# Kernel tuning notes

Hardware: AMD Instinct MI355X
Metric: run time of the kernel (lower is better)

## Reference

```python
import jax, jax.numpy as jnp
import numpy as np

DIM = 1536
NHEADS = 12
HDIM = DIM // NHEADS  # 128
EPS = 1e-6
LOCAL_ATTN_SIZE = 3
SINK_SIZE = 1
MAX_ATTN = 32760 if LOCAL_ATTN_SIZE == -1 else LOCAL_ATTN_SIZE * 1560  # 4680


def _rms(x, g):
    # WanRMSNorm over last dim
    return x * jax.lax.rsqrt(jnp.mean(x * x, axis=-1, keepdims=True) + EPS) * g


def _rope(x, f, h, w, fr, fi, start_frame):
    # x: [b, s, n, d] with s == f*h*w; fr/fi: [1024, d//2] real/imag of complex rotations
    b, s, n, d = x.shape
    c = d // 2
    c0 = c - 2 * (c // 3)
    c1 = c // 3
    fc = jax.lax.complex(fr, fi)  # [1024, c]
    xr = x.reshape(b, s, n, c, 2)
    xc = jax.lax.complex(xr[..., 0], xr[..., 1])  # [b, s, n, c]
    ff = fc[start_frame:start_frame + f, :c0]      # [f, c0]
    fh = fc[:h, c0:c0 + c1]                        # [h, c1]
    fw = fc[:w, c0 + c1:c0 + 2 * c1]               # [w, c1]
    freqs_i = jnp.concatenate([
        jnp.broadcast_to(ff[:, None, None, :], (f, h, w, c0)),
        jnp.broadcast_to(fh[None, :, None, :], (f, h, w, c1)),
        jnp.broadcast_to(fw[None, None, :, :], (f, h, w, c1)),
    ], axis=-1).reshape(1, s, 1, c)
    y = xc * freqs_i
    return jnp.stack([y.real, y.imag], axis=-1).reshape(b, s, n, d)


def _attn(q, k, v):
    # plain SDPA (decode path of the module uses no mask on the gathered window)
    scale = 1.0 / np.sqrt(q.shape[-1]).astype(np.float32)
    logits = jnp.einsum('bqnd,bknd->bnqk', q, k) * scale
    p = jax.nn.softmax(logits, axis=-1)
    return jnp.einsum('bnqk,bknd->bqnd', p, v)


def _forward(x, cache_k, cache_v, freqs_real, freqs_imag,
             wq, bq, wk, bk, wv, bv, wo, bo, gq, gk,
             f_frames, height, width, current_start, global_end_index, local_end_index):
    b, s, _ = x.shape
    n, d = NHEADS, HDIM
    frame_seqlen = height * width
    start_frame = current_start // frame_seqlen

    q = _rms(x @ wq + bq, gq).reshape(b, s, n, d)
    k = _rms(x @ wk + bk, gk).reshape(b, s, n, d)
    v = (x @ wv + bv).reshape(b, s, n, d)

    rq = _rope(q, f_frames, height, width, freqs_real, freqs_imag, start_frame)
    rk = _rope(k, f_frames, height, width, freqs_real, freqs_imag, start_frame)

    current_end = current_start + s
    sink_tokens = SINK_SIZE * frame_seqlen
    kv_size = cache_k.shape[1]
    is_recompute = (current_end <= global_end_index) and (current_start > 0)

    kc, vc = cache_k, cache_v
    if LOCAL_ATTN_SIZE != -1 and current_end > global_end_index and s + local_end_index > kv_size:
        # evict oldest non-sink tokens, roll the rest toward the sink region
        num_evicted = s + local_end_index - kv_size
        num_rolled = local_end_index - num_evicted - sink_tokens
        src = slice(sink_tokens + num_evicted, sink_tokens + num_evicted + num_rolled)
        kc = kc.at[:, sink_tokens:sink_tokens + num_rolled].set(jax.lax.stop_gradient(cache_k[:, src]))
        vc = vc.at[:, sink_tokens:sink_tokens + num_rolled].set(jax.lax.stop_gradient(cache_v[:, src]))
        new_local_end = local_end_index + current_end - global_end_index - num_evicted
    else:
        new_local_end = local_end_index + current_end - global_end_index
    local_start = new_local_end - s
    write_start = max(local_start, sink_tokens) if is_recompute else local_start
    off = max(0, write_start - local_start)
    wl = max(0, new_local_end - write_start)
    if wl > 0:
        kc = kc.at[:, write_start:new_local_end].set(rk[:, off:off + wl])
        vc = vc.at[:, write_start:new_local_end].set(v[:, off:off + wl])

    if sink_tokens > 0:
        budget = MAX_ATTN - sink_tokens
        if budget > 0:
            lo = max(sink_tokens, new_local_end - budget)
            kcat = jnp.concatenate([kc[:, :sink_tokens], kc[:, lo:new_local_end]], axis=1)
            vcat = jnp.concatenate([vc[:, :sink_tokens], vc[:, lo:new_local_end]], axis=1)
        else:
            kcat, vcat = kc[:, :sink_tokens], vc[:, :sink_tokens]
        o = _attn(rq, kcat, vcat)
    else:
        ws = max(0, new_local_end - MAX_ATTN)
        o = _attn(rq, kc[:, ws:new_local_end], vc[:, ws:new_local_end])

    return o.reshape(b, s, DIM) @ wo + bo


def setup_inputs() -> dict:
    key = jax.random.key(0)
    ks = jax.random.split(key, 12)
    B, S, CACHE = 1, 1560, 4680
    sc = 0.02
    # RoPE tables as unit-magnitude complex rotations
    ang = jax.random.uniform(ks[0], (1024, HDIM // 2), jnp.float32, 0.0, 2.0 * np.pi)
    return {
        'x': jax.random.normal(ks[1], (B, S, DIM), jnp.float32),
        'cache_k': jax.random.normal(ks[2], (B, CACHE, NHEADS, HDIM), jnp.float32),
        'cache_v': jax.random.normal(ks[3], (B, CACHE, NHEADS, HDIM), jnp.float32),
        'freqs_real': jnp.cos(ang),
        'freqs_imag': jnp.sin(ang),
        'wq': jax.random.normal(ks[4], (DIM, DIM), jnp.float32) * sc,
        'bq': jnp.zeros((DIM,), jnp.float32),
        'wk': jax.random.normal(ks[5], (DIM, DIM), jnp.float32) * sc,
        'bk': jnp.zeros((DIM,), jnp.float32),
        'wv': jax.random.normal(ks[6], (DIM, DIM), jnp.float32) * sc,
        'bv': jnp.zeros((DIM,), jnp.float32),
        'wo': jax.random.normal(ks[7], (DIM, DIM), jnp.float32) * sc,
        'bo': jnp.zeros((DIM,), jnp.float32),
        'gq': jnp.ones((DIM,), jnp.float32),
        'gk': jnp.ones((DIM,), jnp.float32),
        'f_frames': 1,
        'height': 30,
        'width': 52,
        'current_start': 4680,
        'global_end_index': 4680,
        'local_end_index': 4680,
    }


def reference(x, cache_k, cache_v, freqs_real, freqs_imag,
              wq, bq, wk, bk, wv, bv, wo, bo, gq, gk,
              f_frames, height, width, current_start, global_end_index, local_end_index):
    return _forward(x, cache_k, cache_v, freqs_real, freqs_imag,
                    wq, bq, wk, bk, wv, bv, wo, bo, gq, gk,
                    f_frames, height, width, current_start, global_end_index, local_end_index)
```

## Files before the change

kernel.cpp:

```cpp
#include <hip/hip_runtime.h>
#include <cstdint>
#include <cstddef>

typedef unsigned int  u32;
typedef unsigned short u16;
typedef short s16x8 __attribute__((ext_vector_type(8)));
typedef float f32x4 __attribute__((ext_vector_type(4)));

#define DIM     1536
#define NH      12
#define HD      128
#define SEQ     1560
#define MPAD    1664
#define NKV     4680
#define NKPAD   4736
#define ROLL0   3120
#define NQK     4608
#define START_FRAME 3
#define NEGINF  -3.0e4f
#define NSPLIT  4
#define SPLITKC 1216

__device__ __forceinline__ u16 f2bf(float f){
  u32 u = __builtin_bit_cast(u32, f);
  u32 r = (u + 0x7fffu + ((u >> 16) & 1u)) >> 16;
  return (u16)r;
}

__global__ void k_pre(const float* __restrict__ x, u16* __restrict__ xp,
                      u16* __restrict__ Kc, u16* __restrict__ VT,
                      u16* __restrict__ Qr, u16* __restrict__ Opad,
                      float* __restrict__ sumsq){
  int b = blockIdx.x;
  if (b < 244){
    int i = b * 256 + threadIdx.x;
    uint4 z = make_uint4(0u, 0u, 0u, 0u);
    if (i < 10752){
      int h = i / 896, r = i % 896;
      ((uint4*)(Kc + ((size_t)h * NKPAD + NKV) * 128))[r] = z;
    } else if (i < 21504){
      int j = i - 10752; int row = j / 7, c = j % 7;
      ((uint4*)(VT + (size_t)row * NKPAD + NKV))[c] = z;
    } else if (i < 41472){
      int j = i - 21504; int h = j / 1664, r = j % 1664;
      ((uint4*)(Qr + ((size_t)h * MPAD + SEQ) * 128))[r] = z;
    } else if (i < 61440){
      int r = i - 41472;
      ((uint4*)(Opad + (size_t)SEQ * DIM))[r] = z;
    } else if (i < 62272){
      ((uint4*)sumsq)[i - 61440] = z;
    }
  } else {
    int i = (b - 244) * 256 + threadIdx.x;
    const int n_src = SEQ * DIM / 8;
    u16 o[8] = {0,0,0,0,0,0,0,0};
    if (i < n_src){
      float4 a = ((const float4*)x)[2*i];
      float4 c = ((const float4*)x)[2*i + 1];
      o[0]=f2bf(a.x); o[1]=f2bf(a.y); o[2]=f2bf(a.z); o[3]=f2bf(a.w);
      o[4]=f2bf(c.x); o[5]=f2bf(c.y); o[6]=f2bf(c.z); o[7]=f2bf(c.w);
    }
    uint4 v = make_uint4((u32)o[0]|((u32)o[1]<<16), (u32)o[2]|((u32)o[3]<<16),
                         (u32)o[4]|((u32)o[5]<<16), (u32)o[6]|((u32)o[7]<<16));
    ((uint4*)xp)[i] = v;
  }
}

__global__ void k_transpose_w(const float* __restrict__ wq, const float* __restrict__ wk,
                              const float* __restrict__ wv, const float* __restrict__ wo,
                              u16* __restrict__ WTqkv, u16* __restrict__ WTo){
  __shared__ u32 tile[64][65];
  int z = blockIdx.z;
  const float* w = (z==0)?wq:(z==1)?wk:(z==2)?wv:wo;
  u16* dst = (z < 3) ? (WTqkv + (size_t)z * DIM * DIM) : WTo;
  int r0 = blockIdx.x * 64, c0 = blockIdx.y * 64;
  int t = threadIdx.x;
  int rr = t >> 4, cg = t & 15;
#pragma unroll
  for (int i = 0; i < 4; i++){
    int r = rr + i * 16;
    float4 v = *(const float4*)(w + (size_t)(r0 + r) * DIM + c0 + cg * 4);
    tile[r][cg*4+0] = f2bf(v.x); tile[r][cg*4+1] = f2bf(v.y);
    tile[r][cg*4+2] = f2bf(v.z); tile[r][cg*4+3] = f2bf(v.w);
  }
  __syncthreads();
  int c = t >> 2, rg = t & 3;
  u32 wds[8];
#pragma unroll
  for (int j = 0; j < 8; j++)
    wds[j] = (tile[rg*16 + 2*j][c] & 0xffffu) | (tile[rg*16 + 2*j + 1][c] << 16);
  u16* q = dst + (size_t)(c0 + c) * DIM + r0 + rg * 16;
  *(uint4*)q       = make_uint4(wds[0], wds[1], wds[2], wds[3]);
  *(uint4*)(q + 8) = make_uint4(wds[4], wds[5], wds[6], wds[7]);
}

#define LDK 40
__global__ __launch_bounds__(256) void k_gemm_qkv(
    const u16* __restrict__ A, const u16* __restrict__ B,
    const float* __restrict__ biasq, const float* __restrict__ biask, const float* __restrict__ biasv,
    float* __restrict__ Y, float* __restrict__ sumsq){
  __shared__ u16 As[128*LDK];
  __shared__ u16 Bs[128*LDK];
  int m0 = blockIdx.y * 128, n0 = blockIdx.x * 128;
  int t = threadIdx.x, w = t >> 6, lane = t & 63, quad = lane >> 4, lc = lane & 15;
  int wm = w & 1, wn = w >> 1;
  int sr = t >> 1, sh = (t & 1) * 16;
  f32x4 acc[4][4] = {};
  for (int kt = 0; kt < DIM/32; kt++){
    int k0 = kt * 32;
    __syncthreads();
    {
      const uint4* ga = (const uint4*)(A + (size_t)(m0 + sr) * DIM + k0 + sh);
      uint4 a0 = ga[0], a1 = ga[1];
      const uint4* gb = (const uint4*)(B + (size_t)(n0 + sr) * DIM + k0 + sh);
      uint4 b0 = gb[0], b1 = gb[1];
      *(uint4*)(As + sr * LDK + sh)     = a0;
      *(uint4*)(As + sr * LDK + sh + 8) = a1;
      *(uint4*)(Bs + sr * LDK + sh)     = b0;
      *(uint4*)(Bs + sr * LDK + sh + 8) = b1;
    }
    __syncthreads();
    s16x8 af[4], bf[4];
#pragma unroll
    for (int mt = 0; mt < 4; mt++) af[mt] = *(const s16x8*)(As + (wm*64 + mt*16 + lc) * LDK + quad * 8);
#pragma unroll
    for (int nt = 0; nt < 4; nt++) bf[nt] = *(const s16x8*)(Bs + (wn*64 + nt*16 + lc) * LDK + quad * 8);
#pragma unroll
    for (int mt = 0; mt < 4; mt++)
#pragma unroll
      for (int nt = 0; nt < 4; nt++)
        acc[mt][nt] = __builtin_amdgcn_mfma_f32_16x16x32_bf16(af[mt], bf[nt], acc[mt][nt], 0, 0, 0);
  }
  const float* bias; int cbase; int which;
  if (n0 < DIM)        { bias = biasq; cbase = 0;     which = 0; }
  else if (n0 < 2*DIM) { bias = biask; cbase = DIM;   which = 1; }
  else                 { bias = biasv; cbase = 2*DIM; which = 2; }
  float bvals[4];
#pragma unroll
  for (int nt = 0; nt < 4; nt++) bvals[nt] = bias[n0 - cbase + wn*64 + nt*16 + lc];
#pragma unroll
  for (int mt = 0; mt < 4; mt++){
    int row0 = m0 + wm*64 + mt*16 + quad*4;
    float ss[4] = {0.f, 0.f, 0.f, 0.f};
#pragma unroll
    for (int nt = 0; nt < 4; nt++){
      int col = n0 + wn*64 + nt*16 + lc;
#pragma unroll
      for (int r = 0; r < 4; r++){
        float y = acc[mt][nt][r] + bvals[nt];
        Y[(size_t)(row0 + r) * NQK + col] = y;
        ss[r] += y * y;
      }
    }
    if (which < 2){
      float* dst = sumsq + (which ? MPAD : 0);
#pragma unroll
      for (int r = 0; r < 4; r++){
        float v = ss[r];
        v += __shfl_xor(v, 1); v += __shfl_xor(v, 2); v += __shfl_xor(v, 4); v += __shfl_xor(v, 8);
        if (lc == 0) atomicAdd(&dst[row0 + r], v);
      }
    }
  }
}

__global__ void k_rope_qk(const float* __restrict__ Y, const float* __restrict__ sumsq,
                          const float* __restrict__ gq, const float* __restrict__ gk,
                          const float* __restrict__ fre, const float* __restrict__ fim,
                          u16* __restrict__ Qr, u16* __restrict__ Kc){
  int pos = blockIdx.x;
  int t = threadIdx.x;
  float scq = rsqrtf(sumsq[pos]        * (1.0f/1536.0f) + 1e-6f);
  float sck = rsqrtf(sumsq[MPAD + pos] * (1.0f/1536.0f) + 1e-6f);
  int hrow = pos / 52, wrow = pos % 52;
#pragma unroll
  for (int i = 0; i < 3; i++){
    int p = t + i * 256;
    int head = p >> 6, j = p & 63;
    int frow = (j < 22) ? START_FRAME : ((j < 43) ? hrow : wrow);
    float cr = fre[frow * 64 + j], ci = fim[frow * 64 + j];
    int d0 = head * 128 + 2 * j;
    float2 yq = *(const float2*)(Y + (size_t)pos * NQK + d0);
    float qa = yq.x * scq * gq[d0];
    float qb = yq.y * scq * gq[d0 + 1];
    u32 oq = (u32)f2bf(qa * cr - qb * ci) | ((u32)f2bf(qa * ci + qb * cr) << 16);
    *(u32*)(Qr + (size_t)(head * MPAD + pos) * 128 + 2 * j) = oq;
    float2 yk = *(const float2*)(Y + (size_t)pos * NQK + DIM + d0);
    float ka = yk.x * sck * gk[d0];
    float kb = yk.y * sck * gk[d0 + 1];
    u32 ok = (u32)f2bf(ka * cr - kb * ci) | ((u32)f2bf(ka * ci + kb * cr) << 16);
    *(u32*)(Kc + (size_t)(head * NKPAD + ROLL0 + pos) * 128 + 2 * j) = ok;
  }
}

__global__ void k_copy_cache_k(const float* __restrict__ ck, u16* __restrict__ Kc){
  int p = blockIdx.x;
  int src = (p < SEQ) ? p : p + SEQ;
  int t = threadIdx.x;
  int h = t >> 4, d = (t & 15) * 8;
  const float* s = ck + (size_t)src * DIM + t * 8;
  float4 a = ((const float4*)s)[0], b = ((const float4*)s)[1];
  uint4 v = make_uint4((u32)f2bf(a.x)|((u32)f2bf(a.y)<<16), (u32)f2bf(a.z)|((u32)f2bf(a.w)<<16),
                       (u32)f2bf(b.x)|((u32)f2bf(b.y)<<16), (u32)f2bf(b.z)|((u32)f2bf(b.w)<<16));
  *(uint4*)(Kc + (size_t)(h * NKPAD + p) * 128 + d) = v;
}

__global__ void k_tv_cache(const float* __restrict__ cv, u16* __restrict__ VT){
  __shared__ u32 tile[64][65];
  int p0 = blockIdx.x * 64, hd0 = blockIdx.y * 64;
  int t = threadIdx.x;
  int pr = t >> 4, cg = t & 15;
#pragma unroll
  for (int i = 0; i < 4; i++){
    int p = p0 + pr + i * 16;
    if (p < ROLL0){
      int src = (p < SEQ) ? p : p + SEQ;
      float4 v = *(const float4*)(cv + (size_t)src * DIM + hd0 + cg * 4);
      tile[pr + i*16][cg*4+0] = f2bf(v.x); tile[pr + i*16][cg*4+1] = f2bf(v.y);
      tile[pr + i*16][cg*4+2] = f2bf(v.z); tile[pr + i*16][cg*4+3] = f2bf(v.w);
    }
  }
  __syncthreads();
  int hd = t >> 2, pg = t & 3;
  int pbase = p0 + pg * 16;
  if (pbase < ROLL0){
    u32 wds[8];
#pragma unroll
    for (int j = 0; j < 8; j++)
      wds[j] = (tile[pg*16 + 2*j][hd] & 0xffffu) | (tile[pg*16 + 2*j + 1][hd] << 16);
    u16* q = VT + (size_t)(hd0 + hd) * NKPAD + pbase;
    *(uint4*)q       = make_uint4(wds[0], wds[1], wds[2], wds[3]);
    *(uint4*)(q + 8) = make_uint4(wds[4], wds[5], wds[6], wds[7]);
  }
}

__global__ void k_tv_new(const float* __restrict__ Y, u16* __restrict__ VT){
  __shared__ u32 tile[64][65];
  int p0 = blockIdx.x * 64, hd0 = blockIdx.y * 64;
  int t = threadIdx.x;
  int pr = t >> 4, cg = t & 15;
#pragma unroll
  for (int i = 0; i < 4; i++){
    int p = p0 + pr + i * 16;
    if (p < SEQ){
      float4 v = *(const float4*)(Y + (size_t)p * NQK + 2*DIM + hd0 + cg * 4);
      tile[pr + i*16][cg*4+0] = f2bf(v.x); tile[pr + i*16][cg*4+1] = f2bf(v.y);
      tile[pr + i*16][cg*4+2] = f2bf(v.z); tile[pr + i*16][cg*4+3] = f2bf(v.w);
    }
  }
  __syncthreads();
  int hd = t >> 2, pg = t & 3;
  int pbase = p0 + pg * 16;
  u32 wds[8];
#pragma unroll
  for (int j = 0; j < 8; j++)
    wds[j] = (tile[pg*16 + 2*j][hd] & 0xffffu) | (tile[pg*16 + 2*j + 1][hd] << 16);
  u16* q = VT + (size_t)(hd0 + hd) * NKPAD + ROLL0 + pbase;
  if (pbase + 8  <= SEQ) *(uint4*)q       = make_uint4(wds[0], wds[1], wds[2], wds[3]);
  if (pbase + 16 <= SEQ) *(uint4*)(q + 8) = make_uint4(wds[4], wds[5], wds[6], wds[7]);
}

#define DEFER_THR 8.0f
__global__ __launch_bounds__(512, 4) void k_attn(const u16* __restrict__ Qr, const u16* __restrict__ Kc,
                                                 const u16* __restrict__ VT,
                                                 float* __restrict__ Opart, float* __restrict__ ml){
  __shared__ u16 Ks[64 * 128];
  __shared__ u16 Vs[128 * 64];
  int h = blockIdx.y, qb = blockIdx.x, sp = blockIdx.z;
  int t = threadIdx.x, w = t >> 6, lane = t & 63, quad = lane >> 4, lc = lane & 15;
  int qbase = qb * 128 + w * 16;
  const u16* Qbase = Qr + (size_t)(h * MPAD + qbase + lc) * 128;
  s16x8 qf[4];
#pragma unroll
  for (int kk = 0; kk < 4; kk++) qf[kk] = *(const s16x8*)(Qbase + kk * 32 + quad * 8);
  f32x4 oacc[8] = {};
  float m_ = NEGINF;
  float l_ = 0.f;
  const float scale = 0.08838834764831845f;
  const u16* Kh = Kc + (size_t)h * NKPAD * 128;
  const u16* Vh = VT + (size_t)h * 128 * NKPAD;
  int kr0 = t >> 4,          kg0 = (t & 15) * 8;
  int kr1 = (t + 512) >> 4,  kg1 = ((t + 512) & 15) * 8;
  int vd0 = t >> 3,          vp0 = (t & 7) * 8;
  int vd1 = (t + 512) >> 3,  vp1 = ((t + 512) & 7) * 8;
  int ksw0 = kr0 * 128 + (kg0 ^ ((kr0 & 7) << 3));
  int ksw1 = kr1 * 128 + (kg1 ^ ((kr1 & 7) << 3));
  int vsw0 = vd0 * 64  + (vp0 ^ ((vd0 & 7) << 3));
  int vsw1 = vd1 * 64  + (vp1 ^ ((vd1 & 7) << 3));
  int xork = (lc & 7) << 3;
  int aa = (lc + ((quad & 1) << 5)) << 2;
  int ab = aa + 64;
  int hi = quad >> 1;

  int kc0 = sp * SPLITKC;
  int kc1 = (sp == NSPLIT-1) ? NKPAD : kc0 + SPLITKC;
  uint4 kp0, kp1, vq0, vq1;
  {
    int kc = kc0;
    kp0 = *(const uint4*)(Kh + (size_t)(kc + kr0) * 128 + kg0);
    kp1 = *(const uint4*)(Kh + (size_t)(kc + kr1) * 128 + kg1);
    vq0 = *(const uint4*)(Vh + (size_t)vd0 * NKPAD + kc + vp0);
    vq1 = *(const uint4*)(Vh + (size_t)vd1 * NKPAD + kc + vp1);
  }
  for (int kc = kc0; kc < kc1; kc += 64){
    __syncthreads();
    *(uint4*)(Ks + ksw0) = kp0;
    *(uint4*)(Ks + ksw1) = kp1;
    *(uint4*)(Vs + vsw0) = vq0;
    *(uint4*)(Vs + vsw1) = vq1;
    __syncthreads();
    if (kc + 64 < kc1){
      int kn = kc + 64;
      kp0 = *(const uint4*)(Kh + (size_t)(kn + kr0) * 128 + kg0);
      kp1 = *(const uint4*)(Kh + (size_t)(kn + kr1) * 128 + kg1);
      vq0 = *(const uint4*)(Vh + (size_t)vd0 * NKPAD + kn + vp0);
      vq1 = *(const uint4*)(Vh + (size_t)vd1 * NKPAD + kn + vp1);
    }
    float s[4][4];
    __builtin_amdgcn_s_setprio(1);
#pragma unroll
    for (int nt = 0; nt < 4; nt++){
      f32x4 acc = {};
      int p = nt * 16 + lc;
#pragma unroll
      for (int kk = 0; kk < 4; kk++){
        s16x8 kf = *(const s16x8*)(Ks + p * 128 + (((kk * 4 + quad) * 8) ^ xork));
        acc = __builtin_amdgcn_mfma_f32_16x16x32_bf16(kf, qf[kk], acc, 0, 0, 0);
      }
#pragma unroll
      for (int r = 0; r < 4; r++) s[nt][r] = acc[r] * scale;
    }
    __builtin_amdgcn_s_setprio(0);
    if (kc + 64 > NKV){
#pragma unroll
      for (int nt = 0; nt < 4; nt++){
        int keyb = kc + nt * 16 + quad * 4;
#pragma unroll
        for (int r = 0; r < 4; r++) if (keyb + r >= NKV) s[nt][r] = NEGINF;
      }
    }
    float mx = fmaxf(fmaxf(s[0][0], s[0][1]), fmaxf(s[0][2], s[0][3]));
#pragma unroll
    for (int nt = 1; nt < 4; nt++)
      mx = fmaxf(mx, fmaxf(fmaxf(s[nt][0], s[nt][1]), fmaxf(s[nt][2], s[nt][3])));
    mx = fmaxf(mx, __shfl_xor(mx, 16));
    mx = fmaxf(mx, __shfl_xor(mx, 32));
    if (__any(mx > m_ + DEFER_THR)){
      float mnew = fmaxf(m_, mx);
      float alpha = __expf(m_ - mnew);
      m_ = mnew; l_ *= alpha;
      float alr[4];
#pragma unroll
      for (int r = 0; r < 4; r++) alr[r] = __shfl(alpha, quad * 4 + r);
#pragma unroll
      for (int dt = 0; dt < 8; dt++){
        f32x4 oo = oacc[dt];
#pragma unroll
        for (int r = 0; r < 4; r++) oo[r] *= alr[r];
        oacc[dt] = oo;
      }
    }
#pragma unroll
    for (int nt = 0; nt < 4; nt++)
#pragma unroll
      for (int r = 0; r < 4; r++) s[nt][r] = __expf(s[nt][r] - m_);
    float sum = (s[0][0] + s[0][1]) + (s[0][2] + s[0][3]);
#pragma unroll
    for (int nt = 1; nt < 4; nt++)
      sum += (s[nt][0] + s[nt][1]) + (s[nt][2] + s[nt][3]);
    sum += __shfl_xor(sum, 16);
    sum += __shfl_xor(sum, 32);
    l_ += sum;
    u32 w01[4], w23[4];
#pragma unroll
    for (int nt = 0; nt < 4; nt++){
      w01[nt] = (u32)f2bf(s[nt][0]) | ((u32)f2bf(s[nt][1]) << 16);
      w23[nt] = (u32)f2bf(s[nt][2]) | ((u32)f2bf(s[nt][3]) << 16);
    }
    u32 x0, x1;
    uint4 A0, A1;
    x0 = (u32)__builtin_amdgcn_ds_bpermute(aa, (int)w01[0]);
    x1 = (u32)__builtin_amdgcn_ds_bpermute(aa, (int)w01[1]);
    A0.x = hi ? x1 : x0;
    x0 = (u32)__builtin_amdgcn_ds_bpermute(aa, (int)w23[0]);
    x1 = (u32)__builtin_amdgcn_ds_bpermute(aa, (int)w23[1]);
    A0.y = hi ? x1 : x0;
    x0 = (u32)__builtin_amdgcn_ds_bpermute(ab, (int)w01[0]);
    x1 = (u32)__builtin_amdgcn_ds_bpermute(ab, (int)w01[1]);
    A0.z = hi ? x1 : x0;
    x0 = (u32)__builtin_amdgcn_ds_bpermute(ab, (int)w23[0]);
    x1 = (u32)__builtin_amdgcn_ds_bpermute(ab, (int)w23[1]);
    A0.w = hi ? x1 : x0;
    x0 = (u32)__builtin_amdgcn_ds_bpermute(aa, (int)w01[2]);
    x1 = (u32)__builtin_amdgcn_ds_bpermute(aa, (int)w01[3]);
    A1.x = hi ? x1 : x0;
    x0 = (u32)__builtin_amdgcn_ds_bpermute(aa, (int)w23[2]);
    x1 = (u32)__builtin_amdgcn_ds_bpermute(aa, (int)w23[3]);
    A1.y = hi ? x1 : x0;
    x0 = (u32)__builtin_amdgcn_ds_bpermute(ab, (int)w01[2]);
    x1 = (u32)__builtin_amdgcn_ds_bpermute(ab, (int)w01[3]);
    A1.z = hi ? x1 : x0;
    x0 = (u32)__builtin_amdgcn_ds_bpermute(ab, (int)w23[2]);
    x1 = (u32)__builtin_amdgcn_ds_bpermute(ab, (int)w23[3]);
    A1.w = hi ? x1 : x0;
    s16x8 a0 = __builtin_bit_cast(s16x8, A0);
    s16x8 a1 = __builtin_bit_cast(s16x8, A1);
    __builtin_amdgcn_s_setprio(1);
#pragma unroll
    for (int dt = 0; dt < 8; dt++){
      int d = dt * 16 + lc;
      s16x8 v0 = *(const s16x8*)(Vs + d * 64 + ((quad * 8) ^ xork));
      s16x8 v1 = *(const s16x8*)(Vs + d * 64 + ((32 + quad * 8) ^ xork));
      oacc[dt] = __builtin_amdgcn_mfma_f32_16x16x32_bf16(a0, v0, oacc[dt], 0, 0, 0);
      oacc[dt] = __builtin_amdgcn_mfma_f32_16x16x32_bf16(a1, v1, oacc[dt], 0, 0, 0);
    }
    __builtin_amdgcn_s_setprio(0);
  }
  float mr[4], lr[4];
#pragma unroll
  for (int r = 0; r < 4; r++){
    mr[r] = __shfl(m_, quad * 4 + r);
    lr[r] = __shfl(l_, quad * 4 + r);
  }
  float* Ob = Opart + ((size_t)(sp * NH + h) * SEQ) * 128;
  float* mlb = ml + ((size_t)(sp * NH + h) * SEQ) * 2;
#pragma unroll
  for (int dt = 0; dt < 8; dt++)
#pragma unroll
    for (int r = 0; r < 4; r++){
      int row = qbase + quad * 4 + r;
      if (row < SEQ) Ob[(size_t)row * 128 + dt * 16 + lc] = oacc[dt][r];
    }
  if (lc == 0){
#pragma unroll
    for (int r = 0; r < 4; r++){
      int row = qbase + quad * 4 + r;
      if (row < SEQ){
        mlb[row * 2 + 0] = mr[r];
        mlb[row * 2 + 1] = lr[r];
      }
    }
  }
}

__global__ void k_attn_cmb(const float* __restrict__ Opart, const float* __restrict__ ml,
                           u16* __restrict__ Og){
  int row = blockIdx.x, h = blockIdx.y, d = threadIdx.x;
  float m[NSPLIT], l[NSPLIT];
  float M = NEGINF;
#pragma unroll
  for (int s = 0; s < NSPLIT; s++){
    m[s] = ml[((size_t)(s * NH + h) * SEQ + row) * 2 + 0];
    l[s] = ml[((size_t)(s * NH + h) * SEQ + row) * 2 + 1];
    M = fmaxf(M, m[s]);
  }
  float L = 0.f, o = 0.f;
#pragma unroll
  for (int s = 0; s < NSPLIT; s++){
    float wgt = __expf(m[s] - M);
    L += wgt * l[s];
    o += wgt * Opart[((size_t)(s * NH + h) * SEQ + row) * 128 + d];
  }
  Og[(size_t)row * DIM + h * 128 + d] = f2bf(o / L);
}

__global__ __launch_bounds__(256) void k_gemm_out(const u16* __restrict__ A, const u16* __restrict__ B,
                                                  const float* __restrict__ bo, float* __restrict__ out){
  __shared__ u16 As[128*LDK];
  __shared__ u16 Bs[128*LDK];
  int m0 = blockIdx.y * 128, n0 = blockIdx.x * 128;
  int t = threadIdx.x, w = t >> 6, lane = t & 63, quad = lane >> 4, lc = lane & 15;
  int wm = w & 1, wn = w >> 1;
  int sr = t >> 1, sh = (t & 1) * 16;
  f32x4 acc[4][4] = {};
  for (int kt = 0; kt < DIM/32; kt++){
    int k0 = kt * 32;
    __syncthreads();
    {
      const uint4* ga = (const uint4*)(A + (size_t)(m0 + sr) * DIM + k0 + sh);
      uint4 a0 = ga[0], a1 = ga[1];
      const uint4* gb = (const uint4*)(B + (size_t)(n0 + sr) * DIM + k0 + sh);
      uint4 b0 = gb[0], b1 = gb[1];
      *(uint4*)(As + sr * LDK + sh)     = a0;
      *(uint4*)(As + sr * LDK + sh + 8) = a1;
      *(uint4*)(Bs + sr * LDK + sh)     = b0;
      *(uint4*)(Bs + sr * LDK + sh + 8) = b1;
    }
    __syncthreads();
    s16x8 af[4], bf[4];
#pragma unroll
    for (int mt = 0; mt < 4; mt++) af[mt] = *(const s16x8*)(As + (wm*64 + mt*16 + lc) * LDK + quad * 8);
#pragma unroll
    for (int nt = 0; nt < 4; nt++) bf[nt] = *(const s16x8*)(Bs + (wn*64 + nt*16 + lc) * LDK + quad * 8);
#pragma unroll
    for (int mt = 0; mt < 4; mt++)
#pragma unroll
      for (int nt = 0; nt < 4; nt++)
        acc[mt][nt] = __builtin_amdgcn_mfma_f32_16x16x32_bf16(af[mt], bf[nt], acc[mt][nt], 0, 0, 0);
  }
  float bvals[4];
#pragma unroll
  for (int nt = 0; nt < 4; nt++) bvals[nt] = bo[n0 + wn*64 + nt*16 + lc];
#pragma unroll
  for (int mt = 0; mt < 4; mt++){
    int row0 = m0 + wm*64 + mt*16 + quad*4;
#pragma unroll
    for (int nt = 0; nt < 4; nt++){
      int col = n0 + wn*64 + nt*16 + lc;
#pragma unroll
      for (int r = 0; r < 4; r++){
        int row = row0 + r;
        if (row < SEQ) out[(size_t)row * DIM + col] = acc[mt][nt][r] + bvals[nt];
      }
    }
  }
}

extern "C" void kernel_launch(void* const* d_in, const int* in_sizes, int n_in,
                              void* d_out, int out_size, void* d_ws, size_t ws_size,
                              hipStream_t stream){
  const float* x   = (const float*)d_in[0];
  const float* ck  = (const float*)d_in[1];
  const float* cv  = (const float*)d_in[2];
  const float* fre = (const float*)d_in[3];
  const float* fim = (const float*)d_in[4];
  const float* wq  = (const float*)d_in[5];
  const float* bq  = (const float*)d_in[6];
  const float* wk  = (const float*)d_in[7];
  const float* bk  = (const float*)d_in[8];
  const float* wv  = (const float*)d_in[9];
  const float* bv  = (const float*)d_in[10];
  const float* wo  = (const float*)d_in[11];
  const float* bo  = (const float*)d_in[12];
  const float* gq  = (const float*)d_in[13];
  const float* gk  = (const float*)d_in[14];

  char* ws = (char*)d_ws;
  size_t off = 0;
  u16*   xpad  = (u16*)(ws + off);  off += (size_t)MPAD * DIM * 2;
  u16*   WTqkv = (u16*)(ws + off);  off += (size_t)3 * DIM * DIM * 2;
  float* Y     = (float*)(ws + off); off += (size_t)MPAD * NQK * 4;
  u16*   WTo   = (u16*)(ws + off);  off += (size_t)DIM * DIM * 2;
  float* sumsq = (float*)(ws + off); off += (size_t)2 * MPAD * 4;
  u16*   Qr    = (u16*)(ws + off);  off += (size_t)NH * MPAD * 128 * 2;
  u16*   Kc    = (u16*)(ws + off);  off += (size_t)NH * NKPAD * 128 * 2;
  u16*   VT    = (u16*)(ws + off);  off += (size_t)NH * 128 * NKPAD * 2;
  u16*   Opad  = (u16*)(ws + off);  off += (size_t)MPAD * DIM * 2;
  if (off > ws_size) return;
  float* Opart = (float*)ws;
  float* ml    = (float*)(ws + (size_t)NSPLIT * NH * SEQ * 128 * 4);

  k_pre         <<<dim3(1492), 256, 0, stream>>>(x, xpad, Kc, VT, Qr, Opad, sumsq);
  k_transpose_w <<<dim3(24, 24, 4), 256, 0, stream>>>(wq, wk, wv, wo, WTqkv, WTo);
  k_gemm_qkv    <<<dim3(NQK/128, MPAD/128), 256, 0, stream>>>(xpad, WTqkv, bq, bk, bv, Y, sumsq);
  k_rope_qk     <<<dim3(SEQ), 256, 0, stream>>>(Y, sumsq, gq, gk, fre, fim, Qr, Kc);
  k_copy_cache_k<<<dim3(ROLL0), 192, 0, stream>>>(ck, Kc);
  k_tv_cache    <<<dim3(49, 24), 256, 0, stream>>>(cv, VT);
  k_tv_new      <<<dim3(25, 24), 256, 0, stream>>>(Y, VT);
  k_attn        <<<dim3(MPAD/128, NH, NSPLIT), 512, 0, stream>>>(Qr, Kc, VT, Opart, ml);
  k_attn_cmb    <<<dim3(SEQ, NH), 128, 0, stream>>>(Opart, ml, Opad);
  k_gemm_out    <<<dim3(DIM/128, MPAD/128), 256, 0, stream>>>(Opad, WTo, bo, (float*)d_out);
}
```

Measured before the change: 377.3 us.

## Process two query sub-tiles per wave in attention to reuse K/V fragments

The attention kernel now runs 256 threads per block, and each wave handles 32 query rows as two 16-row sub-tiles (A and B) instead of one. Each K fragment and V fragment read from LDS feeds two MFMAs, which halves LDS reads per MFMA and gives each wave more independent MFMA work. In exchange, accumulator and softmax register state doubles, launch bounds drop to (256,2), and each block stages its K/V tile with half as many threads. Occupancy falls and register spills become a risk.

After: 519.7 us. 37.8% more time.

```diff
diff --git a/kernel.cpp b/kernel.cpp
--- a/kernel.cpp
+++ b/kernel.cpp
@@ -261,32 +261,38 @@
 }
 
 #define DEFER_THR 8.0f
-__global__ __launch_bounds__(512, 4) void k_attn(const u16* __restrict__ Qr, const u16* __restrict__ Kc,
+__global__ __launch_bounds__(256, 2) void k_attn(const u16* __restrict__ Qr, const u16* __restrict__ Kc,
                                                  const u16* __restrict__ VT,
                                                  float* __restrict__ Opart, float* __restrict__ ml){
   __shared__ u16 Ks[64 * 128];
   __shared__ u16 Vs[128 * 64];
   int h = blockIdx.y, qb = blockIdx.x, sp = blockIdx.z;
   int t = threadIdx.x, w = t >> 6, lane = t & 63, quad = lane >> 4, lc = lane & 15;
-  int qbase = qb * 128 + w * 16;
-  const u16* Qbase = Qr + (size_t)(h * MPAD + qbase + lc) * 128;
-  s16x8 qf[4];
-#pragma unroll
-  for (int kk = 0; kk < 4; kk++) qf[kk] = *(const s16x8*)(Qbase + kk * 32 + quad * 8);
-  f32x4 oacc[8] = {};
-  float m_ = NEGINF;
-  float l_ = 0.f;
+  int qbaseA = qb * 128 + w * 32;
+  int qbaseB = qbaseA + 16;
+  const u16* QbA = Qr + (size_t)(h * MPAD + qbaseA + lc) * 128;
+  const u16* QbB = Qr + (size_t)(h * MPAD + qbaseB + lc) * 128;
+  s16x8 qfA[4], qfB[4];
+#pragma unroll
+  for (int kk = 0; kk < 4; kk++){
+    qfA[kk] = *(const s16x8*)(QbA + kk * 32 + quad * 8);
+    qfB[kk] = *(const s16x8*)(QbB + kk * 32 + quad * 8);
+  }
+  f32x4 oaccA[8] = {}, oaccB[8] = {};
+  float mA = NEGINF, lA = 0.f;
+  float mB = NEGINF, lB = 0.f;
   const float scale = 0.08838834764831845f;
   const u16* Kh = Kc + (size_t)h * NKPAD * 128;
   const u16* Vh = VT + (size_t)h * 128 * NKPAD;
-  int kr0 = t >> 4,          kg0 = (t & 15) * 8;
-  int kr1 = (t + 512) >> 4,  kg1 = ((t + 512) & 15) * 8;
-  int vd0 = t >> 3,          vp0 = (t & 7) * 8;
-  int vd1 = (t + 512) >> 3,  vp1 = ((t + 512) & 7) * 8;
-  int ksw0 = kr0 * 128 + (kg0 ^ ((kr0 & 7) << 3));
-  int ksw1 = kr1 * 128 + (kg1 ^ ((kr1 & 7) << 3));
-  int vsw0 = vd0 * 64  + (vp0 ^ ((vd0 & 7) << 3));
-  int vsw1 = vd1 * 64  + (vp1 ^ ((vd1 & 7) << 3));
+  int kr[4], kg[4], ksw[4], vd[4], vp[4], vsw[4];
+#pragma unroll
+  for (int i = 0; i < 4; i++){
+    int n = t + i * 256;
+    kr[i] = n >> 4;  kg[i] = (n & 15) * 8;
+    ksw[i] = kr[i] * 128 + (kg[i] ^ ((kr[i] & 7) << 3));
+    vd[i] = n >> 3;  vp[i] = (n & 7) * 8;
+    vsw[i] = vd[i] * 64 + (vp[i] ^ ((vd[i] & 7) << 3));
+  }
   int xork = (lc & 7) << 3;
   int aa = (lc + ((quad & 1) << 5)) << 2;
   int ab = aa + 64;
@@ -294,41 +300,45 @@
 
   int kc0 = sp * SPLITKC;
   int kc1 = (sp == NSPLIT-1) ? NKPAD : kc0 + SPLITKC;
-  uint4 kp0, kp1, vq0, vq1;
-  {
-    int kc = kc0;
-    kp0 = *(const uint4*)(Kh + (size_t)(kc + kr0) * 128 + kg0);
-    kp1 = *(const uint4*)(Kh + (size_t)(kc + kr1) * 128 + kg1);
-    vq0 = *(const uint4*)(Vh + (size_t)vd0 * NKPAD + kc + vp0);
-    vq1 = *(const uint4*)(Vh + (size_t)vd1 * NKPAD + kc + vp1);
+  uint4 kp[4], vq[4];
+#pragma unroll
+  for (int i = 0; i < 4; i++){
+    kp[i] = *(const uint4*)(Kh + (size_t)(kc0 + kr[i]) * 128 + kg[i]);
+    vq[i] = *(const uint4*)(Vh + (size_t)vd[i] * NKPAD + kc0 + vp[i]);
   }
   for (int kc = kc0; kc < kc1; kc += 64){
     __syncthreads();
-    *(uint4*)(Ks + ksw0) = kp0;
-    *(uint4*)(Ks + ksw1) = kp1;
-    *(uint4*)(Vs + vsw0) = vq0;
-    *(uint4*)(Vs + vsw1) = vq1;
+#pragma unroll
+    for (int i = 0; i < 4; i++){
+      *(uint4*)(Ks + ksw[i]) = kp[i];
+      *(uint4*)(Vs + vsw[i]) = vq[i];
+    }
     __syncthreads();
     if (kc + 64 < kc1){
       int kn = kc + 64;
-      kp0 = *(const uint4*)(Kh + (size_t)(kn + kr0) * 128 + kg0);
-      kp1 = *(const uint4*)(Kh + (size_t)(kn + kr1) * 128 + kg1);
-      vq0 = *(const uint4*)(Vh + (size_t)vd0 * NKPAD + kn + vp0);
-      vq1 = *(const uint4*)(Vh + (size_t)vd1 * NKPAD + kn + vp1);
-    }
-    float s[4][4];
+#pragma unroll
+      for (int i = 0; i < 4; i++){
+        kp[i] = *(const uint4*)(Kh + (size_t)(kn + kr[i]) * 128 + kg[i]);
+        vq[i] = *(const uint4*)(Vh + (size_t)vd[i] * NKPAD + kn + vp[i]);
+      }
+    }
+    float sA[4][4], sB[4][4];
     __builtin_amdgcn_s_setprio(1);
 #pragma unroll
     for (int nt = 0; nt < 4; nt++){
-      f32x4 acc = {};
+      f32x4 accA = {}, accB = {};
       int p = nt * 16 + lc;
 #pragma unroll
       for (int kk = 0; kk < 4; kk++){
         s16x8 kf = *(const s16x8*)(Ks + p * 128 + (((kk * 4 + quad) * 8) ^ xork));
-        acc = __builtin_amdgcn_mfma_f32_16x16x32_bf16(kf, qf[kk], acc, 0, 0, 0);
-      }
-#pragma unroll
-      for (int r = 0; r < 4; r++) s[nt][r] = acc[r] * scale;
+        accA = __builtin_amdgcn_mfma_f32_16x16x32_bf16(kf, qfA[kk], accA, 0, 0, 0);
+        accB = __builtin_amdgcn_mfma_f32_16x16x32_bf16(kf, qfB[kk], accB, 0, 0, 0);
+      }
+#pragma unroll
+      for (int r = 0; r < 4; r++){
+        sA[nt][r] = accA[r] * scale;
+        sB[nt][r] = accB[r] * scale;
+      }
     }
     __builtin_amdgcn_s_setprio(0);
     if (kc + 64 > NKV){
@@ -336,91 +346,136 @@
       for (int nt = 0; nt < 4; nt++){
         int keyb = kc + nt * 16 + quad * 4;
 #pragma unroll
-        for (int r = 0; r < 4; r++) if (keyb + r >= NKV) s[nt][r] = NEGINF;
-      }
-    }
-    float mx = fmaxf(fmaxf(s[0][0], s[0][1]), fmaxf(s[0][2], s[0][3]));
-#pragma unroll
-    for (int nt = 1; nt < 4; nt++)
-      mx = fmaxf(mx, fmaxf(fmaxf(s[nt][0], s[nt][1]), fmaxf(s[nt][2], s[nt][3])));
-    mx = fmaxf(mx, __shfl_xor(mx, 16));
-    mx = fmaxf(mx, __shfl_xor(mx, 32));
-    if (__any(mx > m_ + DEFER_THR)){
-      float mnew = fmaxf(m_, mx);
-      float alpha = __expf(m_ - mnew);
-      m_ = mnew; l_ *= alpha;
-      float alr[4];
-#pragma unroll
-      for (int r = 0; r < 4; r++) alr[r] = __shfl(alpha, quad * 4 + r);
+        for (int r = 0; r < 4; r++)
+          if (keyb + r >= NKV){ sA[nt][r] = NEGINF; sB[nt][r] = NEGINF; }
+      }
+    }
+    float mxA = fmaxf(fmaxf(sA[0][0], sA[0][1]), fmaxf(sA[0][2], sA[0][3]));
+    float mxB = fmaxf(fmaxf(sB[0][0], sB[0][1]), fmaxf(sB[0][2], sB[0][3]));
+#pragma unroll
+    for (int nt = 1; nt < 4; nt++){
+      mxA = fmaxf(mxA, fmaxf(fmaxf(sA[nt][0], sA[nt][1]), fmaxf(sA[nt][2], sA[nt][3])));
+      mxB = fmaxf(mxB, fmaxf(fmaxf(sB[nt][0], sB[nt][1]), fmaxf(sB[nt][2], sB[nt][3])));
+    }
+    mxA = fmaxf(mxA, __shfl_xor(mxA, 16));  mxB = fmaxf(mxB, __shfl_xor(mxB, 16));
+    mxA = fmaxf(mxA, __shfl_xor(mxA, 32));  mxB = fmaxf(mxB, __shfl_xor(mxB, 32));
+    if (__any((mxA > mA + DEFER_THR) || (mxB > mB + DEFER_THR))){
+      float mnA = fmaxf(mA, mxA), mnB = fmaxf(mB, mxB);
+      float alA = __expf(mA - mnA), alB = __expf(mB - mnB);
+      mA = mnA; lA *= alA;  mB = mnB; lB *= alB;
+      float arA[4], arB[4];
+#pragma unroll
+      for (int r = 0; r < 4; r++){
+        arA[r] = __shfl(alA, quad * 4 + r);
+        arB[r] = __shfl(alB, quad * 4 + r);
+      }
 #pragma unroll
       for (int dt = 0; dt < 8; dt++){
-        f32x4 oo = oacc[dt];
-#pragma unroll
-        for (int r = 0; r < 4; r++) oo[r] *= alr[r];
-        oacc[dt] = oo;
+        f32x4 oA = oaccA[dt], oB = oaccB[dt];
+#pragma unroll
+        for (int r = 0; r < 4; r++){ oA[r] *= arA[r]; oB[r] *= arB[r]; }
+        oaccA[dt] = oA; oaccB[dt] = oB;
       }
     }
 #pragma unroll
     for (int nt = 0; nt < 4; nt++)
 #pragma unroll
-      for (int r = 0; r < 4; r++) s[nt][r] = __expf(s[nt][r] - m_);
-    float sum = (s[0][0] + s[0][1]) + (s[0][2] + s[0][3]);
-#pragma unroll
-    for (int nt = 1; nt < 4; nt++)
-      sum += (s[nt][0] + s[nt][1]) + (s[nt][2] + s[nt][3]);
-    sum += __shfl_xor(sum, 16);
-    sum += __shfl_xor(sum, 32);
-    l_ += sum;
-    u32 w01[4], w23[4];
+      for (int r = 0; r < 4; r++){
+        sA[nt][r] = __expf(sA[nt][r] - mA);
+        sB[nt][r] = __expf(sB[nt][r] - mB);
+      }
+    float smA = (sA[0][0] + sA[0][1]) + (sA[0][2] + sA[0][3]);
+    float smB = (sB[0][0] + sB[0][1]) + (sB[0][2] + sB[0][3]);
+#pragma unroll
+    for (int nt = 1; nt < 4; nt++){
+      smA += (sA[nt][0] + sA[nt][1]) + (sA[nt][2] + sA[nt][3]);
+      smB += (sB[nt][0] + sB[nt][1]) + (sB[nt][2] + sB[nt][3]);
+    }
+    smA += __shfl_xor(smA, 16);  smB += __shfl_xor(smB, 16);
+    smA += __shfl_xor(smA, 32);  smB += __shfl_xor(smB, 32);
+    lA += smA;  lB += smB;
+    u32 a01[4], a23[4], b01[4], b23[4];
 #pragma unroll
     for (int nt = 0; nt < 4; nt++){
-      w01[nt] = (u32)f2bf(s[nt][0]) | ((u32)f2bf(s[nt][1]) << 16);
-      w23[nt] = (u32)f2bf(s[nt][2]) | ((u32)f2bf(s[nt][3]) << 16);
+      a01[nt] = (u32)f2bf(sA[nt][0]) | ((u32)f2bf(sA[nt][1]) << 16);
+      a23[nt] = (u32)f2bf(sA[nt][2]) | ((u32)f2bf(sA[nt][3]) << 16);
+      b01[nt] = (u32)f2bf(sB[nt][0]) | ((u32)f2bf(sB[nt][1]) << 16);
+      b23[nt] = (u32)f2bf(sB[nt][2]) | ((u32)f2bf(sB[nt][3]) << 16);
     }
     u32 x0, x1;
-    uint4 A0, A1;
-    x0 = (u32)__builtin_amdgcn_ds_bpermute(aa, (int)w01[0]);
-    x1 = (u32)__builtin_amdgcn_ds_bpermute(aa, (int)w01[1]);
+    uint4 A0, A1, B0, B1;
+    x0 = (u32)__builtin_amdgcn_ds_bpermute(aa, (int)a01[0]);
+    x1 = (u32)__builtin_amdgcn_ds_bpermute(aa, (int)a01[1]);
     A0.x = hi ? x1 : x0;
-    x0 = (u32)__builtin_amdgcn_ds_bpermute(aa, (int)w23[0]);
-    x1 = (u32)__builtin_amdgcn_ds_bpermute(aa, (int)w23[1]);
+    x0 = (u32)__builtin_amdgcn_ds_bpermute(aa, (int)a23[0]);
+    x1 = (u32)__builtin_amdgcn_ds_bpermute(aa, (int)a23[1]);
     A0.y = hi ? x1 : x0;
-    x0 = (u32)__builtin_amdgcn_ds_bpermute(ab, (int)w01[0]);
-    x1 = (u32)__builtin_amdgcn_ds_bpermute(ab, (int)w01[1]);
+    x0 = (u32)__builtin_amdgcn_ds_bpermute(ab, (int)a01[0]);
+    x1 = (u32)__builtin_amdgcn_ds_bpermute(ab, (int)a01[1]);
     A0.z = hi ? x1 : x0;
-    x0 = (u32)__builtin_amdgcn_ds_bpermute(ab, (int)w23[0]);
-    x1 = (u32)__builtin_amdgcn_ds_bpermute(ab, (int)w23[1]);
+    x0 = (u32)__builtin_amdgcn_ds_bpermute(ab, (int)a23[0]);
+    x1 = (u32)__builtin_amdgcn_ds_bpermute(ab, (int)a23[1]);
     A0.w = hi ? x1 : x0;
-    x0 = (u32)__builtin_amdgcn_ds_bpermute(aa, (int)w01[2]);
-    x1 = (u32)__builtin_amdgcn_ds_bpermute(aa, (int)w01[3]);
+    x0 = (u32)__builtin_amdgcn_ds_bpermute(aa, (int)a01[2]);
+    x1 = (u32)__builtin_amdgcn_ds_bpermute(aa, (int)a01[3]);
     A1.x = hi ? x1 : x0;
-    x0 = (u32)__builtin_amdgcn_ds_bpermute(aa, (int)w23[2]);
-    x1 = (u32)__builtin_amdgcn_ds_bpermute(aa, (int)w23[3]);
+    x0 = (u32)__builtin_amdgcn_ds_bpermute(aa, (int)a23[2]);
+    x1 = (u32)__builtin_amdgcn_ds_bpermute(aa, (int)a23[3]);
     A1.y = hi ? x1 : x0;
-    x0 = (u32)__builtin_amdgcn_ds_bpermute(ab, (int)w01[2]);
-    x1 = (u32)__builtin_amdgcn_ds_bpermute(ab, (int)w01[3]);
+    x0 = (u32)__builtin_amdgcn_ds_bpermute(ab, (int)a01[2]);
+    x1 = (u32)__builtin_amdgcn_ds_bpermute(ab, (int)a01[3]);
     A1.z = hi ? x1 : x0;
-    x0 = (u32)__builtin_amdgcn_ds_bpermute(ab, (int)w23[2]);
-    x1 = (u32)__builtin_amdgcn_ds_bpermute(ab, (int)w23[3]);
+    x0 = (u32)__builtin_amdgcn_ds_bpermute(ab, (int)a23[2]);
+    x1 = (u32)__builtin_amdgcn_ds_bpermute(ab, (int)a23[3]);
     A1.w = hi ? x1 : x0;
+    x0 = (u32)__builtin_amdgcn_ds_bpermute(aa, (int)b01[0]);
+    x1 = (u32)__builtin_amdgcn_ds_bpermute(aa, (int)b01[1]);
+    B0.x = hi ? x1 : x0;
+    x0 = (u32)__builtin_amdgcn_ds_bpermute(aa, (int)b23[0]);
+    x1 = (u32)__builtin_amdgcn_ds_bpermute(aa, (int)b23[1]);
+    B0.y = hi ? x1 : x0;
+    x0 = (u32)__builtin_amdgcn_ds_bpermute(ab, (int)b01[0]);
+    x1 = (u32)__builtin_amdgcn_ds_bpermute(ab, (int)b01[1]);
+    B0.z = hi ? x1 : x0;
+    x0 = (u32)__builtin_amdgcn_ds_bpermute(ab, (int)b23[0]);
+    x1 = (u32)__builtin_amdgcn_ds_bpermute(ab, (int)b23[1]);
+    B0.w = hi ? x1 : x0;
+    x0 = (u32)__builtin_amdgcn_ds_bpermute(aa, (int)b01[2]);
+    x1 = (u32)__builtin_amdgcn_ds_bpermute(aa, (int)b01[3]);
+    B1.x = hi ? x1 : x0;
+    x0 = (u32)__builtin_amdgcn_ds_bpermute(aa, (int)b23[2]);
+    x1 = (u32)__builtin_amdgcn_ds_bpermute(aa, (int)b23[3]);
+    B1.y = hi ? x1 : x0;
+    x0 = (u32)__builtin_amdgcn_ds_bpermute(ab, (int)b01[2]);
+    x1 = (u32)__builtin_amdgcn_ds_bpermute(ab, (int)b01[3]);
+    B1.z = hi ? x1 : x0;
+    x0 = (u32)__builtin_amdgcn_ds_bpermute(ab, (int)b23[2]);
+    x1 = (u32)__builtin_amdgcn_ds_bpermute(ab, (int)b23[3]);
+    B1.w = hi ? x1 : x0;
     s16x8 a0 = __builtin_bit_cast(s16x8, A0);
     s16x8 a1 = __builtin_bit_cast(s16x8, A1);
+    s16x8 b0 = __builtin_bit_cast(s16x8, B0);
+    s16x8 b1 = __builtin_bit_cast(s16x8, B1);
     __builtin_amdgcn_s_setprio(1);
 #pragma unroll
     for (int dt = 0; dt < 8; dt++){
       int d = dt * 16 + lc;
       s16x8 v0 = *(const s16x8*)(Vs + d * 64 + ((quad * 8) ^ xork));
       s16x8 v1 = *(const s16x8*)(Vs + d * 64 + ((32 + quad * 8) ^ xork));
-      oacc[dt] = __builtin_amdgcn_mfma_f32_16x16x32_bf16(a0, v0, oacc[dt], 0, 0, 0);
-      oacc[dt] = __builtin_amdgcn_mfma_f32_16x16x32_bf16(a1, v1, oacc[dt], 0, 0, 0);
+      oaccA[dt] = __builtin_amdgcn_mfma_f32_16x16x32_bf16(a0, v0, oaccA[dt], 0, 0, 0);
+      oaccB[dt] = __builtin_amdgcn_mfma_f32_16x16x32_bf16(b0, v0, oaccB[dt], 0, 0, 0);
+      oaccA[dt] = __builtin_amdgcn_mfma_f32_16x16x32_bf16(a1, v1, oaccA[dt], 0, 0, 0);
+      oaccB[dt] = __builtin_amdgcn_mfma_f32_16x16x32_bf16(b1, v1, oaccB[dt], 0, 0, 0);
     }
     __builtin_amdgcn_s_setprio(0);
   }
-  float mr[4], lr[4];
+  float mrA[4], lrA[4], mrB[4], lrB[4];
 #pragma unroll
   for (int r = 0; r < 4; r++){
-    mr[r] = __shfl(m_, quad * 4 + r);
-    lr[r] = __shfl(l_, quad * 4 + r);
+    mrA[r] = __shfl(mA, quad * 4 + r);
+    lrA[r] = __shfl(lA, quad * 4 + r);
+    mrB[r] = __shfl(mB, quad * 4 + r);
+    lrB[r] = __shfl(lB, quad * 4 + r);
   }
   float* Ob = Opart + ((size_t)(sp * NH + h) * SEQ) * 128;
   float* mlb = ml + ((size_t)(sp * NH + h) * SEQ) * 2;
@@ -428,16 +483,23 @@
   for (int dt = 0; dt < 8; dt++)
 #pragma unroll
     for (int r = 0; r < 4; r++){
-      int row = qbase + quad * 4 + r;
-      if (row < SEQ) Ob[(size_t)row * 128 + dt * 16 + lc] = oacc[dt][r];
+      int rowA = qbaseA + quad * 4 + r;
+      int rowB = qbaseB + quad * 4 + r;
+      if (rowA < SEQ) Ob[(size_t)rowA * 128 + dt * 16 + lc] = oaccA[dt][r];
+      if (rowB < SEQ) Ob[(size_t)rowB * 128 + dt * 16 + lc] = oaccB[dt][r];
     }
   if (lc == 0){
 #pragma unroll
     for (int r = 0; r < 4; r++){
-      int row = qbase + quad * 4 + r;
-      if (row < SEQ){
-        mlb[row * 2 + 0] = mr[r];
-        mlb[row * 2 + 1] = lr[r];
+      int rowA = qbaseA + quad * 4 + r;
+      int rowB = qbaseB + quad * 4 + r;
+      if (rowA < SEQ){
+        mlb[rowA * 2 + 0] = mrA[r];
+        mlb[rowA * 2 + 1] = lrA[r];
+      }
+      if (rowB < SEQ){
+        mlb[rowB * 2 + 0] = mrB[r];
+        mlb[rowB * 2 + 1] = lrB[r];
       }
     }
   }
@@ -557,7 +619,7 @@
   k_copy_cache_k<<<dim3(ROLL0), 192, 0, stream>>>(ck, Kc);
   k_tv_cache    <<<dim3(49, 24), 256, 0, stream>>>(cv, VT);
   k_tv_new      <<<dim3(25, 24), 256, 0, stream>>>(Y, VT);
-  k_attn        <<<dim3(MPAD/128, NH, NSPLIT), 512, 0, stream>>>(Qr, Kc, VT, Opart, ml);
+  k_attn        <<<dim3(MPAD/128, NH, NSPLIT), 256, 0, stream>>>(Qr, Kc, VT, Opart, ml);
   k_attn_cmb    <<<dim3(SEQ, NH), 128, 0, stream>>>(Opart, ml, Opad);
   k_gemm_out    <<<dim3(DIM/128, MPAD/128), 256, 0, stream>>>(Opad, WTo, bo, (float*)d_out);
 }
```
